# Kernel optimization log

Hardware: AMD Instinct MI355X
Metric: run time of the kernel (lower is better)

Reference implementation:

```python
import jax, jax.numpy as jnp
import numpy as np
from jax import lax

B, H, W = 32, 40, 256
FREQ = 40            # freq_num
WIND = 0.5           # wind_size (seconds)
KF = 5               # input_filter_kernel (odd -> 'same' length)
CNN_OUT = 64 * 36 * 252  # out_channels[-1] * (H-4) * (W-4)


def setup_inputs() -> dict:
    key = jax.random.key(0)
    ks = jax.random.split(key, 9)
    return {
        "inputs": jax.random.normal(ks[0], (B, 1, H, W), jnp.float32),
        "w0": jax.random.normal(ks[1], (32, 1, 3, 3), jnp.float32) * 0.1,
        "b0": jax.random.normal(ks[2], (32,), jnp.float32) * 0.05,
        "w1": jax.random.normal(ks[3], (64, 32, 3, 3), jnp.float32) * 0.05,
        "b1": jax.random.normal(ks[4], (64,), jnp.float32) * 0.05,
        "wf": jax.random.normal(ks[5], (1, 1, 1, KF), jnp.float32) * 0.2,
        "bf": jax.random.normal(ks[6], (1,), jnp.float32) * 0.05,
        "wr": jax.random.normal(ks[7], (FREQ, CNN_OUT), jnp.float32) * 1e-3,
        "br": jax.random.normal(ks[8], (FREQ,), jnp.float32) * 0.05,
    }


def _conv2d(x, w, padding):
    return lax.conv_general_dilated(
        x, w, window_strides=(1, 1), padding=padding,
        dimension_numbers=("NCHW", "OIHW", "NCHW"))


def reference(inputs, w0, b0, w1, b1, wf, bf, wr, br):
    b, _, h, w_len = inputs.shape
    # input_filter: Conv1d(1,1,KF, padding=KF//2) applied independently per
    # frequency row -> equivalent to a 2D conv with a (1,KF) kernel.
    p = KF // 2
    feats = _conv2d(inputs, wf, [(0, 0), (p, p)]) + bf[None, :, None, None]  # [B,1,H,W]

    # conv stack with ReLU
    x = jax.nn.relu(_conv2d(inputs, w0, "VALID") + b0[None, :, None, None])
    x = jax.nn.relu(_conv2d(x, w1, "VALID") + b1[None, :, None, None])

    gates = jax.nn.sigmoid(x.reshape(b, -1) @ wr.T + br)

    fs = (1.0 / WIND) * jnp.linspace(1.0, FREQ, FREQ)          # [FREQ]
    wtd_mean_mod = jnp.mean(gates * fs[None, :])               # scalar

    # Fused modulation transform: instead of the per-frequency python loop
    # with materialized [B,H,W] broadcasts, compute sin/cos bases [FREQ,W]
    # and reduce over time with a single einsum each.
    t = jnp.linspace(0.0, WIND, w_len)                          # [W]
    phase = (2.0 * np.pi) * fs[:, None] * t[None, :]            # [FREQ,W]
    f0 = feats[:, 0]                                            # [B,H,W]
    inv_w = jnp.float32(1.0 / w_len)
    sins = jnp.einsum("fw,bhw->bfh", jnp.sin(phase), f0) * inv_w  # mean over W
    coss = jnp.einsum("fw,bhw->bfh", jnp.cos(phase), f0) * inv_w
    mag = jnp.sqrt(sins * sins + coss * coss)                   # [B,FREQ,H]
    mods = (mag * gates[:, :, None]).reshape(b, FREQ * h)       # cat over freq, dim=1
    return mods, wtd_mean_mod
```

## Files before the change

### kernel.cpp

```cpp
#include <hip/hip_runtime.h>
#include <hip/hip_bf16.h>
#include <math.h>

#define BB   32
#define HH   40
#define WW   256
#define NF   40
#define H1N  36
#define W1N  252
#define KCNN 580608
#define NBLK2 504
#define KPW  288
#define NREP 32

typedef __attribute__((ext_vector_type(8))) short bf16x8;
typedef __attribute__((ext_vector_type(4))) short bf16x4;
typedef __attribute__((ext_vector_type(4))) float f32x4;

static __device__ __forceinline__ unsigned short f2bf(float v) {
    __hip_bfloat16 h = __float2bfloat16(v);
    return *(unsigned short*)&h;
}

static __device__ __forceinline__ bf16x8 packbf(float4 lo, float4 hi) {
    bf16x8 r;
    r[0] = (short)f2bf(lo.x); r[1] = (short)f2bf(lo.y);
    r[2] = (short)f2bf(lo.z); r[3] = (short)f2bf(lo.w);
    r[4] = (short)f2bf(hi.x); r[5] = (short)f2bf(hi.y);
    r[6] = (short)f2bf(hi.z); r[7] = (short)f2bf(hi.w);
    return r;
}

__global__ void k0_prep(const float* __restrict__ w1, const float* __restrict__ w0,
                        unsigned short* __restrict__ w1c, unsigned short* __restrict__ w0c,
                        float* __restrict__ gaccR, unsigned int* __restrict__ done) {
    int o = blockIdx.x * 256 + threadIdx.x;
    {
        int c0  = o & 31;
        int c1  = (o >> 5) & 63;
        int tap = o >> 11;
        w1c[o] = f2bf(w1[(c1 * 32 + c0) * 9 + tap]);
    }
    if (blockIdx.x >= 40) {
        int rep = blockIdx.x - 40;
        for (int p = threadIdx.x; p < 1280; p += 256) gaccR[rep * 1280 + p] = 0.0f;
    }
    if (blockIdx.x == 70) {
        for (int i = threadIdx.x; i < 1024; i += 256) {
            int c0 = i >> 5, k = i & 31;
            w0c[i] = (k < 9) ? f2bf(w0[c0 * 9 + k]) : (unsigned short)0;
        }
    }
    if (blockIdx.x == 71 && threadIdx.x == 0) *done = 0u;
}

__global__ __launch_bounds__(256) void k1_conv(
        const float* __restrict__ inp, const unsigned short* __restrict__ w0c,
        const float* __restrict__ b0, const unsigned short* __restrict__ w1c,
        const float* __restrict__ b1, unsigned short* __restrict__ xbf) {
    __shared__ __align__(16) unsigned short smem[18432];
    unsigned short* y0T = smem;
    float* ins = (float*)(smem + 16000);
    unsigned short* xp = smem;

    const int jt = blockIdx.x;
    const int it = blockIdx.y;
    const int b  = blockIdx.z;
    const int i0 = it * 4;
    const int j0 = jt * 64;
    const int tid = threadIdx.x;

    const int w    = tid >> 6;
    const int lane = tid & 63;
    const int l15  = lane & 15;
    const int quad = lane >> 4;

    for (int s = tid; s < 546; s += 256) {
        int r = s / 68, c = s - r * 68;
        float v = 0.0f;
        if (r < 8 && (j0 + c) < WW) v = inp[(b * HH + i0 + r) * WW + j0 + c];
        ins[s] = v;
    }
    __syncthreads();

    {
        bf16x8 a0f = *(const bf16x8*)(w0c + (0 * 16 + l15) * 32 + quad * 8);
        bf16x8 a1f = *(const bf16x8*)(w0c + (1 * 16 + l15) * 32 + quad * 8);
        float bias0[2][4];
        #pragma unroll
        for (int mt = 0; mt < 2; ++mt)
            #pragma unroll
            for (int rg = 0; rg < 4; ++rg)
                bias0[mt][rg] = b0[mt * 16 + quad * 4 + rg];

        for (int nt = w; nt < 25; nt += 4) {
            const int pos  = l15 + 16 * nt;
            const int posc = (pos < 396) ? pos : 395;
            const int r    = posc / 66;
            const int col  = posc - r * 66;
            bf16x8 bfrag = (bf16x8){0, 0, 0, 0, 0, 0, 0, 0};
            if (quad == 0) {
                const float* p0 = ins + r * 68 + col;
                bfrag[0] = (short)f2bf(p0[0]);
                bfrag[1] = (short)f2bf(p0[1]);
                bfrag[2] = (short)f2bf(p0[2]);
                bfrag[3] = (short)f2bf(p0[68]);
                bfrag[4] = (short)f2bf(p0[69]);
                bfrag[5] = (short)f2bf(p0[70]);
                bfrag[6] = (short)f2bf(p0[136]);
                bfrag[7] = (short)f2bf(p0[137]);
            } else if (quad == 1) {
                bfrag[0] = (short)f2bf(ins[(r + 2) * 68 + col + 2]);
            }
            f32x4 d0 = (f32x4){0.f, 0.f, 0.f, 0.f};
            f32x4 d1 = (f32x4){0.f, 0.f, 0.f, 0.f};
            d0 = __builtin_amdgcn_mfma_f32_16x16x32_bf16(a0f, bfrag, d0, 0, 0, 0);
            d1 = __builtin_amdgcn_mfma_f32_16x16x32_bf16(a1f, bfrag, d1, 0, 0, 0);
            const bool valid = (j0 + col) < 254;
            if (pos < 396) {
                bf16x4 v0, v1;
                #pragma unroll
                for (int rg = 0; rg < 4; ++rg) {
                    float x0 = valid ? fmaxf(d0[rg] + bias0[0][rg], 0.0f) : 0.0f;
                    float x1 = valid ? fmaxf(d1[rg] + bias0[1][rg], 0.0f) : 0.0f;
                    v0[rg] = (short)f2bf(x0);
                    v1[rg] = (short)f2bf(x1);
                }
                *(bf16x4*)(y0T + pos * 40 +      quad * 4) = v0;
                *(bf16x4*)(y0T + pos * 40 + 16 + quad * 4) = v1;
            }
        }
    }
    __syncthreads();

    float biasr[4][4];
    #pragma unroll
    for (int mt = 0; mt < 4; ++mt)
        #pragma unroll
        for (int rg = 0; rg < 4; ++rg)
            biasr[mt][rg] = b1[mt * 16 + quad * 4 + rg];

    f32x4 acc[4][4];
    #pragma unroll
    for (int mt = 0; mt < 4; ++mt)
        #pragma unroll
        for (int nt = 0; nt < 4; ++nt)
            acc[mt][nt] = (f32x4){0.f, 0.f, 0.f, 0.f};

    #pragma unroll
    for (int ki = 0; ki < 3; ++ki) {
        #pragma unroll
        for (int kj = 0; kj < 3; ++kj) {
            const int tap = ki * 3 + kj;
            bf16x8 af[4], bfr[4];
            #pragma unroll
            for (int mt = 0; mt < 4; ++mt)
                af[mt] = *(const bf16x8*)(w1c + ((tap * 64 + mt * 16 + l15) * 32 + quad * 8));
            #pragma unroll
            for (int nt = 0; nt < 4; ++nt)
                bfr[nt] = *(const bf16x8*)(y0T + (((w + ki) * 66 + nt * 16 + l15 + kj) * 40 + quad * 8));
            #pragma unroll
            for (int mt = 0; mt < 4; ++mt)
                #pragma unroll
                for (int nt = 0; nt < 4; ++nt)
                    acc[mt][nt] = __builtin_amdgcn_mfma_f32_16x16x32_bf16(
                        af[mt], bfr[nt], acc[mt][nt], 0, 0, 0);
        }
    }
    __syncthreads();

    #pragma unroll
    for (int nt = 0; nt < 4; ++nt) {
        const int j = nt * 16 + l15;
        #pragma unroll
        for (int mt = 0; mt < 4; ++mt) {
            #pragma unroll
            for (int rg = 0; rg < 4; ++rg) {
                const int c1 = mt * 16 + quad * 4 + rg;
                const float v = fmaxf(acc[mt][nt][rg] + biasr[mt][rg], 0.0f);
                xp[(c1 * 4 + w) * 72 + j] = f2bf(v);
            }
        }
    }
    __syncthreads();
    {
        const int chunk = tid & 7;
        const int rb    = tid >> 3;
        #pragma unroll
        for (int p = 0; p < 8; ++p) {
            const int rowid = rb + 32 * p;
            const int c1 = rowid >> 2, ci = rowid & 3;
            uint4 v = *(const uint4*)&xp[rowid * 72 + chunk * 8];
            const int gj = j0 + chunk * 8;
            unsigned short* gp = xbf + (size_t)b * KCNN
                               + (size_t)(c1 * H1N + i0 + ci) * W1N + gj;
            uint2 lo; lo.x = v.x; lo.y = v.y;
            if (gj + 8 <= W1N) {
                uint2 hi; hi.x = v.z; hi.y = v.w;
                *(uint2*)gp = lo;
                *(uint2*)(gp + 4) = hi;
            } else if (gj < W1N) {
                *(uint2*)gp = lo;
            }
        }
    }
}

__global__ __launch_bounds__(256) void k2_gemm(
        const unsigned short* __restrict__ xbf, const float* __restrict__ wr,
        const float* __restrict__ br, float* __restrict__ gaccR,
        unsigned int* __restrict__ done, float* __restrict__ gates,
        float* __restrict__ out) {
    __shared__ float red[4][32][41];
    __shared__ unsigned int lastf;

    const int tid  = threadIdx.x;
    const int wv   = tid >> 6;
    const int lane = tid & 63;
    const int l15  = lane & 15;
    const int quad = lane >> 4;
    const size_t kw = (size_t)(blockIdx.x * 4 + wv) * KPW;

    const unsigned short* ap0 = xbf + (size_t)l15 * KCNN + kw + quad * 8;
    const unsigned short* ap1 = ap0 + (size_t)16 * KCNN;
    const float* bp0 = wr + (size_t)l15 * KCNN + kw + quad * 8;
    const float* bp1 = bp0 + (size_t)16 * KCNN;
    const int r2 = (l15 < 8) ? (32 + l15) : 39;
    const float* bp2 = wr + (size_t)r2 * KCNN + kw + quad * 8;

    f32x4 acc[2][3];
    #pragma unroll
    for (int mt = 0; mt < 2; ++mt)
        #pragma unroll
        for (int nt = 0; nt < 3; ++nt)
            acc[mt][nt] = (f32x4){0.f, 0.f, 0.f, 0.f};

    bf16x8 a0c, a1c, a0n, a1n;
    float4 bw[3][2], bwn[3][2];

    a0c = *(const bf16x8*)ap0;
    a1c = *(const bf16x8*)ap1;
    bw[0][0] = *(const float4*)bp0; bw[0][1] = *(const float4*)(bp0 + 4);
    bw[1][0] = *(const float4*)bp1; bw[1][1] = *(const float4*)(bp1 + 4);
    bw[2][0] = *(const float4*)bp2; bw[2][1] = *(const float4*)(bp2 + 4);

    for (int c = 0; c < 9; ++c) {
        if (c < 8) {
            const int o2 = (c + 1) * 32;
            a0n = *(const bf16x8*)(ap0 + o2);
            a1n = *(const bf16x8*)(ap1 + o2);
            bwn[0][0] = *(const float4*)(bp0 + o2); bwn[0][1] = *(const float4*)(bp0 + o2 + 4);
            bwn[1][0] = *(const float4*)(bp1 + o2); bwn[1][1] = *(const float4*)(bp1 + o2 + 4);
            bwn[2][0] = *(const float4*)(bp2 + o2); bwn[2][1] = *(const float4*)(bp2 + o2 + 4);
        }
        #pragma unroll
        for (int nt = 0; nt < 3; ++nt) {
            bf16x8 bfrag = packbf(bw[nt][0], bw[nt][1]);
            acc[0][nt] = __builtin_amdgcn_mfma_f32_16x16x32_bf16(a0c, bfrag, acc[0][nt], 0, 0, 0);
            acc[1][nt] = __builtin_amdgcn_mfma_f32_16x16x32_bf16(a1c, bfrag, acc[1][nt], 0, 0, 0);
        }
        if (c < 8) {
            a0c = a0n; a1c = a1n;
            #pragma unroll
            for (int nt = 0; nt < 3; ++nt) { bw[nt][0] = bwn[nt][0]; bw[nt][1] = bwn[nt][1]; }
        }
    }

    #pragma unroll
    for (int mt = 0; mt < 2; ++mt)
        #pragma unroll
        for (int nt = 0; nt < 3; ++nt)
            #pragma unroll
            for (int rg = 0; rg < 4; ++rg) {
                int bb = mt * 16 + quad * 4 + rg;
                int ff = nt * 16 + l15;
                if (ff < NF) red[wv][bb][ff] = acc[mt][nt][rg];
            }
    __syncthreads();
    float* grep = gaccR + (blockIdx.x & (NREP - 1)) * 1280;
    for (int p = tid; p < 1280; p += 256) {
        int bb = p / 40, ff = p - bb * 40;
        atomicAdd(grep + p, red[0][bb][ff] + red[1][bb][ff] + red[2][bb][ff] + red[3][bb][ff]);
    }
    __syncthreads();

    if (tid == 0) {
        __threadfence();
        lastf = (atomicAdd(done, 1u) == NBLK2 - 1) ? 1u : 0u;
    }
    __syncthreads();
    if (lastf) {
        __threadfence();
        float part = 0.0f;
        for (int p = tid; p < 1280; p += 256) {
            float s = 0.0f;
            #pragma unroll 4
            for (int r = 0; r < NREP; ++r)
                s += __hip_atomic_load(gaccR + r * 1280 + p,
                                       __ATOMIC_RELAXED, __HIP_MEMORY_SCOPE_AGENT);
            int f = p % 40;
            float g = 1.0f / (1.0f + __expf(-(s + br[f])));
            gates[p] = g;
            part += g * 2.0f * (float)(f + 1);
        }
        #pragma unroll
        for (int off = 32; off >= 1; off >>= 1) part += __shfl_xor(part, off);
        float* redf = (float*)red;
        if ((tid & 63) == 0) redf[tid >> 6] = part;
        __syncthreads();
        if (tid == 0)
            out[51200] = (redf[0] + redf[1] + redf[2] + redf[3]) * (1.0f / 1280.0f);
    }
}

__global__ __launch_bounds__(320) void k4_mods(
        const float* __restrict__ inp, const float* __restrict__ wf,
        const float* __restrict__ bfp, const float* __restrict__ gates,
        float* __restrict__ out) {
    const int f = blockIdx.x, b = blockIdx.y;
    const int tid = threadIdx.x;
    const int h  = tid >> 3;
    const int wl = tid & 7;
    float wfv[5];
    #pragma unroll
    for (int t = 0; t < 5; ++t) wfv[t] = wf[t];
    const float bias = bfp[0];
    const float cph = 6.283185307179586f * (float)(f + 1) / 255.0f;
    const float* row = inp + (b * HH + h) * WW;
    float sa = 0.0f, ca = 0.0f;
    for (int m = 0; m < 32; ++m) {
        int w = wl + 8 * m;
        float feat = bias;
        #pragma unroll
        for (int d = -2; d <= 2; ++d) {
            int wc = w + d;
            if (wc >= 0 && wc < WW) feat = fmaf(row[wc], wfv[d + 2], feat);
        }
        float sv, cv;
        __sincosf(cph * (float)w, &sv, &cv);
        sa = fmaf(sv, feat, sa);
        ca = fmaf(cv, feat, ca);
    }
    #pragma unroll
    for (int off = 4; off >= 1; off >>= 1) {
        sa += __shfl_xor(sa, off, 8);
        ca += __shfl_xor(ca, off, 8);
    }
    if (wl == 0) {
        float mag = sqrtf(sa * sa + ca * ca) * (1.0f / 256.0f);
        out[b * 1600 + f * 40 + h] = mag * gates[b * 40 + f];
    }
}

extern "C" void kernel_launch(void* const* d_in, const int* in_sizes, int n_in,
                              void* d_out, int out_size, void* d_ws, size_t ws_size,
                              hipStream_t stream) {
    const float* inp = (const float*)d_in[0];
    const float* w0  = (const float*)d_in[1];
    const float* b0  = (const float*)d_in[2];
    const float* w1  = (const float*)d_in[3];
    const float* b1  = (const float*)d_in[4];
    const float* wf  = (const float*)d_in[5];
    const float* bf_ = (const float*)d_in[6];
    const float* wr  = (const float*)d_in[7];
    const float* br  = (const float*)d_in[8];
    float* out = (float*)d_out;

    char* ws = (char*)d_ws;
    unsigned short* xbf = (unsigned short*)ws;
    unsigned short* w1c = (unsigned short*)(ws + 37158912);
    unsigned short* w0c = (unsigned short*)(ws + 37195776);
    float* gaccR = (float*)(ws + 37197824);
    float* gates = (float*)(ws + 37361664);
    unsigned int* done = (unsigned int*)(ws + 37366784);

    k0_prep<<<72, 256, 0, stream>>>(w1, w0, w1c, w0c, gaccR, done);
    k1_conv<<<dim3(4, 9, 32), 256, 0, stream>>>(inp, w0c, b0, w1c, b1, xbf);
    k2_gemm<<<NBLK2, 256, 0, stream>>>(xbf, wr, br, gaccR, done, gates, out);
    k4_mods<<<dim3(40, 32), 320, 0, stream>>>(inp, wf, bf_, gates, out);
}
```

Baseline: 252.4 us.

## Stage GEMM operands via direct global-to-LDS loads and transpose partial-sum shards

```diff
diff --git a/kernel.cpp b/kernel.cpp
--- a/kernel.cpp
+++ b/kernel.cpp
@@ -29,6 +29,12 @@
     r[4] = (short)f2bf(hi.x); r[5] = (short)f2bf(hi.y);
     r[6] = (short)f2bf(hi.z); r[7] = (short)f2bf(hi.w);
     return r;
+}
+
+static __device__ __forceinline__ void gld16(const void* g, void* l) {
+    __builtin_amdgcn_global_load_lds(
+        (const __attribute__((address_space(1))) void*)g,
+        (__attribute__((address_space(3))) void*)l, 16, 0, 0);
 }
 
 __global__ void k0_prep(const float* __restrict__ w1, const float* __restrict__ w0,
@@ -211,6 +217,7 @@
         const float* __restrict__ br, float* __restrict__ gaccR,
         unsigned int* __restrict__ done, float* __restrict__ gates,
         float* __restrict__ out) {
+    __shared__ __align__(16) unsigned char stg[4][8192];
     __shared__ float red[4][32][41];
     __shared__ unsigned int lastf;
 
@@ -228,6 +235,8 @@
     const int r2 = (l15 < 8) ? (32 + l15) : 39;
     const float* bp2 = wr + (size_t)r2 * KCNN + kw + quad * 8;
 
+    unsigned char* sb = stg[wv];
+
     f32x4 acc[2][3];
     #pragma unroll
     for (int mt = 0; mt < 2; ++mt)
@@ -235,35 +244,36 @@
         for (int nt = 0; nt < 3; ++nt)
             acc[mt][nt] = (f32x4){0.f, 0.f, 0.f, 0.f};
 
-    bf16x8 a0c, a1c, a0n, a1n;
-    float4 bw[3][2], bwn[3][2];
-
-    a0c = *(const bf16x8*)ap0;
-    a1c = *(const bf16x8*)ap1;
-    bw[0][0] = *(const float4*)bp0; bw[0][1] = *(const float4*)(bp0 + 4);
-    bw[1][0] = *(const float4*)bp1; bw[1][1] = *(const float4*)(bp1 + 4);
-    bw[2][0] = *(const float4*)bp2; bw[2][1] = *(const float4*)(bp2 + 4);
-
     for (int c = 0; c < 9; ++c) {
-        if (c < 8) {
-            const int o2 = (c + 1) * 32;
-            a0n = *(const bf16x8*)(ap0 + o2);
-            a1n = *(const bf16x8*)(ap1 + o2);
-            bwn[0][0] = *(const float4*)(bp0 + o2); bwn[0][1] = *(const float4*)(bp0 + o2 + 4);
-            bwn[1][0] = *(const float4*)(bp1 + o2); bwn[1][1] = *(const float4*)(bp1 + o2 + 4);
-            bwn[2][0] = *(const float4*)(bp2 + o2); bwn[2][1] = *(const float4*)(bp2 + o2 + 4);
-        }
-        #pragma unroll
-        for (int nt = 0; nt < 3; ++nt) {
-            bf16x8 bfrag = packbf(bw[nt][0], bw[nt][1]);
-            acc[0][nt] = __builtin_amdgcn_mfma_f32_16x16x32_bf16(a0c, bfrag, acc[0][nt], 0, 0, 0);
-            acc[1][nt] = __builtin_amdgcn_mfma_f32_16x16x32_bf16(a1c, bfrag, acc[1][nt], 0, 0, 0);
-        }
-        if (c < 8) {
-            a0c = a0n; a1c = a1n;
-            #pragma unroll
-            for (int nt = 0; nt < 3; ++nt) { bw[nt][0] = bwn[nt][0]; bw[nt][1] = bwn[nt][1]; }
-        }
+        const int o = c * 32;
+        gld16(ap0 + o, sb);
+        gld16(ap1 + o, sb + 1024);
+        gld16(bp0 + o,     sb + 2048);
+        gld16(bp0 + o + 4, sb + 3072);
+        gld16(bp1 + o,     sb + 4096);
+        gld16(bp1 + o + 4, sb + 5120);
+        gld16(bp2 + o,     sb + 6144);
+        gld16(bp2 + o + 4, sb + 7168);
+        __syncthreads();
+
+        bf16x8 a0 = *(const bf16x8*)(sb +        lane * 16);
+        bf16x8 a1 = *(const bf16x8*)(sb + 1024 + lane * 16);
+        float4 b0l = *(const float4*)(sb + 2048 + lane * 16);
+        float4 b0h = *(const float4*)(sb + 3072 + lane * 16);
+        float4 b1l = *(const float4*)(sb + 4096 + lane * 16);
+        float4 b1h = *(const float4*)(sb + 5120 + lane * 16);
+        float4 b2l = *(const float4*)(sb + 6144 + lane * 16);
+        float4 b2h = *(const float4*)(sb + 7168 + lane * 16);
+
+        bf16x8 f0 = packbf(b0l, b0h);
+        bf16x8 f1 = packbf(b1l, b1h);
+        bf16x8 f2 = packbf(b2l, b2h);
+        acc[0][0] = __builtin_amdgcn_mfma_f32_16x16x32_bf16(a0, f0, acc[0][0], 0, 0, 0);
+        acc[1][0] = __builtin_amdgcn_mfma_f32_16x16x32_bf16(a1, f0, acc[1][0], 0, 0, 0);
+        acc[0][1] = __builtin_amdgcn_mfma_f32_16x16x32_bf16(a0, f1, acc[0][1], 0, 0, 0);
+        acc[1][1] = __builtin_amdgcn_mfma_f32_16x16x32_bf16(a1, f1, acc[1][1], 0, 0, 0);
+        acc[0][2] = __builtin_amdgcn_mfma_f32_16x16x32_bf16(a0, f2, acc[0][2], 0, 0, 0);
+        acc[1][2] = __builtin_amdgcn_mfma_f32_16x16x32_bf16(a1, f2, acc[1][2], 0, 0, 0);
     }
 
     #pragma unroll
@@ -277,10 +287,11 @@
                 if (ff < NF) red[wv][bb][ff] = acc[mt][nt][rg];
             }
     __syncthreads();
-    float* grep = gaccR + (blockIdx.x & (NREP - 1)) * 1280;
+    const int shard = blockIdx.x & (NREP - 1);
     for (int p = tid; p < 1280; p += 256) {
         int bb = p / 40, ff = p - bb * 40;
-        atomicAdd(grep + p, red[0][bb][ff] + red[1][bb][ff] + red[2][bb][ff] + red[3][bb][ff]);
+        atomicAdd(gaccR + (size_t)p * NREP + shard,
+                  red[0][bb][ff] + red[1][bb][ff] + red[2][bb][ff] + red[3][bb][ff]);
     }
     __syncthreads();
 
@@ -293,11 +304,13 @@
         __threadfence();
         float part = 0.0f;
         for (int p = tid; p < 1280; p += 256) {
+            const float4* q = (const float4*)(gaccR + (size_t)p * NREP);
             float s = 0.0f;
-            #pragma unroll 4
-            for (int r = 0; r < NREP; ++r)
-                s += __hip_atomic_load(gaccR + r * 1280 + p,
-                                       __ATOMIC_RELAXED, __HIP_MEMORY_SCOPE_AGENT);
+            #pragma unroll
+            for (int r8 = 0; r8 < 8; ++r8) {
+                float4 v = q[r8];
+                s += (v.x + v.y) + (v.z + v.w);
+            }
             int f = p % 40;
             float g = 1.0f / (1.0f + __expf(-(s + br[f])));
             gates[p] = g;
```

New measurement: 256.2 us. Within noise of the previous version (+1.5%).
